# Optimization experiments

Measured on AMD Instinct MI355X. Metric: run time of the kernel, lower is better.

## Reference

```python
import jax, jax.numpy as jnp
import numpy as np

B, S, H = 2, 2048, 2048
N_HEADS = 16
HEAD_DIM = H // N_HEADS  # 128


def apply_rotary(x, cos, sin):
    # x: (B, n_heads, S, head_dim); cos/sin: (S, head_dim//2)
    d = x.shape[-1] // 2
    x1, x2 = x[..., :d], x[..., d:]
    c = cos[None, None, :x.shape[2]]
    s = sin[None, None, :x.shape[2]]
    return jnp.concatenate([x1 * c - x2 * s, x2 * c + x1 * s], axis=-1)


def setup_inputs() -> dict:
    key = jax.random.key(0)
    k1, k2, k3 = jax.random.split(key, 3)
    x = jax.random.normal(k1, (B, S, H), dtype=jnp.float32)
    qkv_w = jax.random.normal(k2, (3 * H, H), dtype=jnp.float32) * (1.0 / np.sqrt(H))
    o_w = jax.random.normal(k3, (H, H), dtype=jnp.float32) * (1.0 / np.sqrt(H))
    # rotary tables, half head_dim
    inv_freq = 1.0 / (10000.0 ** (jnp.arange(0, HEAD_DIM // 2, dtype=jnp.float32) / (HEAD_DIM // 2)))
    t = jnp.arange(S, dtype=jnp.float32)
    freqs = jnp.outer(t, inv_freq)  # (S, head_dim//2)
    cos, sin = jnp.cos(freqs), jnp.sin(freqs)
    # True = masked (strictly upper triangular)
    causal_mask = jnp.triu(jnp.ones((S, S), dtype=bool), k=1)
    return {"x": x, "qkv_w": qkv_w, "o_w": o_w, "cos": cos, "sin": sin,
            "causal_mask": causal_mask}


def reference(x, qkv_w, o_w, cos, sin, causal_mask):
    Bx, Sx, Hx = x.shape
    qkv = jnp.einsum('bsh,oh->bso', x, qkv_w)  # (B,S,3H)
    qkv = qkv.reshape(Bx, Sx, 3, N_HEADS, HEAD_DIM)
    q, k, v = qkv[:, :, 0], qkv[:, :, 1], qkv[:, :, 2]
    q = jnp.transpose(q, (0, 2, 1, 3))  # (B,nh,S,hd)
    k = jnp.transpose(k, (0, 2, 1, 3))
    v = jnp.transpose(v, (0, 2, 1, 3))
    q = apply_rotary(q, cos, sin)
    k = apply_rotary(k, cos, sin)
    scale = 1.0 / jnp.sqrt(jnp.asarray(HEAD_DIM, dtype=x.dtype))
    attn = jnp.einsum('bnqd,bnkd->bnqk', q, k) * scale
    attn = jnp.where(causal_mask[None, None], -jnp.inf, attn)
    attn = jax.nn.softmax(attn, axis=-1)
    out = jnp.einsum('bnqk,bnkd->bnqd', attn, v)
    out = jnp.transpose(out, (0, 2, 1, 3)).reshape(Bx, Sx, Hx)
    return jnp.einsum('bsh,oh->bso', out, o_w)
```

## Files before the change

kernel.cpp:

```cpp
#include <hip/hip_runtime.h>
#include <hip/hip_bf16.h>
#include <stdint.h>

typedef __attribute__((ext_vector_type(4))) float f32x4;
typedef __attribute__((ext_vector_type(8))) short s16x8;
typedef __attribute__((ext_vector_type(4))) short s16x4;

#define SWZ(g, row) ((((g) & ~7) | (((g) ^ ((row) & 7)) & 7)))

__device__ __forceinline__ unsigned short f2bf(float f) {
  unsigned u = __builtin_bit_cast(unsigned, f);
  u += 0x7fffu + ((u >> 16) & 1u);
  return (unsigned short)(u >> 16);
}

__device__ __forceinline__ void gld16(const void* g, void* l) {
  __builtin_amdgcn_global_load_lds(
      (const __attribute__((address_space(1))) void*)g,
      (__attribute__((address_space(3))) void*)l, 16, 0, 0);
}

__global__ void cvt_f32_to_bf16(const float* __restrict__ src,
                                unsigned short* __restrict__ dst, int n4) {
  int i = blockIdx.x * blockDim.x + threadIdx.x;
  if (i >= n4) return;
  float4 v = ((const float4*)src)[i];
  s16x4 o;
  o[0] = (short)f2bf(v.x); o[1] = (short)f2bf(v.y);
  o[2] = (short)f2bf(v.z); o[3] = (short)f2bf(v.w);
  ((s16x4*)dst)[i] = o;
}

#define STG(ORG, LDSB, HALF, KT) \
  gld16((const char*)((ORG) + ((size_t)((HALF)*128 + srow)) * 2048 + (size_t)(KT) * 64) + gsw, (LDSB) + (HALF) * 16384 + wid * 2048); \
  gld16((const char*)((ORG) + ((size_t)((HALF)*128 + srow + 8)) * 2048 + (size_t)(KT) * 64) + gsw, (LDSB) + (HALF) * 16384 + wid * 2048 + 1024);

#define PH(MQ, NQ, ENDWAIT, ...) \
  { s16x8 af[4][2], bv[2][2]; \
    _Pragma("unroll") for (int j = 0; j < 4; ++j) { \
      const int ra = (MQ)*128 + wm*64 + j*16 + lg; \
      _Pragma("unroll") for (int ks = 0; ks < 2; ++ks) \
        af[j][ks] = *(const s16x8*)(sAc + ra*128 + (((ks*4+hg)^(ra&7)) << 4)); } \
    _Pragma("unroll") for (int j2 = 0; j2 < 2; ++j2) { \
      const int rb = (NQ)*128 + wn*16 + j2*64 + lg; \
      _Pragma("unroll") for (int ks = 0; ks < 2; ++ks) \
        bv[j2][ks] = *(const s16x8*)(sBc + rb*128 + (((ks*4+hg)^(rb&7)) << 4)); } \
    __VA_ARGS__ \
    __builtin_amdgcn_s_barrier(); \
    asm volatile("s_waitcnt lgkmcnt(0)" ::: "memory"); \
    __builtin_amdgcn_sched_barrier(0); \
    __builtin_amdgcn_s_setprio(1); \
    _Pragma("unroll") for (int j = 0; j < 4; ++j) \
      _Pragma("unroll") for (int j2 = 0; j2 < 2; ++j2) \
        _Pragma("unroll") for (int ks = 0; ks < 2; ++ks) \
          acc[(MQ)*4+j][(NQ)*2+j2] = __builtin_amdgcn_mfma_f32_16x16x32_bf16( \
              af[j][ks], bv[j2][ks], acc[(MQ)*4+j][(NQ)*2+j2], 0, 0, 0); \
    __builtin_amdgcn_s_setprio(0); \
    ENDWAIT \
    __builtin_amdgcn_s_barrier(); }

__global__ __launch_bounds__(512, 1) void gemm_qkv_256(
    const unsigned short* __restrict__ A,
    const unsigned short* __restrict__ Bt,
    const float* __restrict__ cosT, const float* __restrict__ sinT,
    unsigned short* __restrict__ qOut, unsigned short* __restrict__ kOut,
    unsigned short* __restrict__ vtOut)
{
  __shared__ char smem[131072];
  const int tid = (int)threadIdx.x;
  const int wid = tid >> 6, l = tid & 63;
  const int lg = l & 15, hg = l >> 4;
  const int wm = wid >> 2, wn = wid & 3;
  const int s = ((int)blockIdx.x & 7) * 48 + ((int)blockIdx.x >> 3);
  const int bm0 = (s & 15) * 256, bn0 = (s >> 4) * 256;

  const int srow = wid * 16 + (l >> 3);
  const int gsw = ((l & 7) ^ (l >> 3)) << 4;

  const unsigned short* Aorg = A + (size_t)bm0 * 2048;
  const unsigned short* Borg = Bt + (size_t)bn0 * 2048;

  f32x4 acc[8][4] = {};

  STG(Aorg, smem + 0, 0, 0)
  STG(Borg, smem + 32768, 0, 0)
  STG(Borg, smem + 32768, 1, 0)
  STG(Aorg, smem + 0, 1, 0)
  asm volatile("s_waitcnt vmcnt(4)" ::: "memory");
  __builtin_amdgcn_s_barrier();

  for (int t = 0; t < 31; ++t) {
    const char* sAc = smem + (t & 1) * 65536;
    const char* sBc = sAc + 32768;
    char* dA = smem + (((t & 1) ^ 1) * 65536);
    char* dB = dA + 32768;
    PH(0, 0, asm volatile("s_waitcnt vmcnt(4)" ::: "memory");, STG(Aorg, dA, 0, t + 1))
    PH(0, 1, asm volatile("s_waitcnt vmcnt(4)" ::: "memory");, STG(Borg, dB, 0, t + 1))
    PH(1, 0, , STG(Borg, dB, 1, t + 1))
    PH(1, 1, asm volatile("s_waitcnt vmcnt(4)" ::: "memory");, STG(Aorg, dA, 1, t + 1))
  }
  {
    const char* sAc = smem + 65536;
    const char* sBc = sAc + 32768;
    PH(0, 0, asm volatile("s_waitcnt vmcnt(2)" ::: "memory");, )
    PH(0, 1, asm volatile("s_waitcnt vmcnt(0)" ::: "memory");, )
    PH(1, 0, , )
    PH(1, 1, , )
  }

  #pragma unroll
  for (int a = 0; a < 8; ++a) {
    const int gr0 = bm0 + (a >> 2) * 128 + wm * 64 + (a & 3) * 16 + hg * 4;
    #pragma unroll
    for (int pb = 0; pb < 2; ++pb) {
      const int obase = bn0 + pb * 128;
      const int tt = obase >> 11;
      const int h = (obase >> 7) & 15;
      const int d = wn * 16 + lg;
      if (tt < 2) {
        unsigned short* dst = (tt == 0) ? qOut : kOut;
        #pragma unroll
        for (int r = 0; r < 4; ++r) {
          const int gr = gr0 + r;
          const int b = gr >> 11, s1 = gr & 2047;
          const float x1 = acc[a][pb * 2 + 0][r];
          const float x2 = acc[a][pb * 2 + 1][r];
          const float cv = cosT[s1 * 64 + d];
          const float sv = sinT[s1 * 64 + d];
          const size_t base = (((size_t)b * 16 + h) * 2048 + s1) * 128;
          dst[base + d]      = f2bf(x1 * cv - x2 * sv);
          dst[base + d + 64] = f2bf(x2 * cv + x1 * sv);
        }
      } else {
        const int b = gr0 >> 11, s0 = gr0 & 2047;
        s16x4 p1, p2;
        #pragma unroll
        for (int r = 0; r < 4; ++r) {
          p1[r] = (short)f2bf(acc[a][pb * 2 + 0][r]);
          p2[r] = (short)f2bf(acc[a][pb * 2 + 1][r]);
        }
        *(s16x4*)(vtOut + (((size_t)b * 16 + h) * 128 + d)      * 2048 + s0) = p1;
        *(s16x4*)(vtOut + (((size_t)b * 16 + h) * 128 + d + 64) * 2048 + s0) = p2;
      }
    }
  }
}

template<int EPI>
__global__ __launch_bounds__(256) void gemm_bt(
    const unsigned short* __restrict__ A,
    const unsigned short* __restrict__ Bt,
    float* __restrict__ C, int N, int K)
{
  __shared__ char smem[32768];
  const int tid = (int)threadIdx.x;
  const int w  = tid >> 6, l = tid & 63;
  const int lg = l & 15, hg = l >> 4;
  const int bn0 = (int)blockIdx.x * 128, bm0 = (int)blockIdx.y * 128;

  f32x4 acc[2][8] = {};
  const int nkt = K >> 6;
  for (int kt = 0; kt < nkt; ++kt) {
    __syncthreads();
    for (int i = 0; i < 4; ++i) {
      const int G = w * 256 + i * 64 + l;
      const int row = G >> 3, g = G & 7;
      const int gs = SWZ(g, row);
      gld16((const char*)(A  + (size_t)(bm0 + row) * K + (size_t)kt * 64) + (gs << 4),
            smem + w * 4096 + i * 1024);
      gld16((const char*)(Bt + (size_t)(bn0 + row) * K + (size_t)kt * 64) + (gs << 4),
            smem + 16384 + w * 4096 + i * 1024);
    }
    asm volatile("s_waitcnt vmcnt(0)" ::: "memory");
    __syncthreads();
    for (int ks = 0; ks < 2; ++ks) {
      s16x8 af[2], bfr[8];
      for (int ai = 0; ai < 2; ++ai) {
        const int ra = w * 32 + ai * 16 + lg;
        const int gr = SWZ(4 * ks + hg, ra);
        af[ai] = *(const s16x8*)(smem + ra * 128 + (gr << 4));
      }
      for (int bi = 0; bi < 8; ++bi) {
        const int rb = bi * 16 + lg;
        const int gr = SWZ(4 * ks + hg, rb);
        bfr[bi] = *(const s16x8*)(smem + 16384 + rb * 128 + (gr << 4));
      }
      for (int ai = 0; ai < 2; ++ai)
        for (int bi = 0; bi < 8; ++bi)
          acc[ai][bi] = __builtin_amdgcn_mfma_f32_16x16x32_bf16(
              af[ai], bfr[bi], acc[ai][bi], 0, 0, 0);
    }
  }

  for (int ai = 0; ai < 2; ++ai)
    for (int bi = 0; bi < 8; ++bi) {
      const int col  = bn0 + bi * 16 + lg;
      const int row0 = bm0 + w * 32 + ai * 16 + hg * 4;
      for (int r = 0; r < 4; ++r)
        C[(size_t)(row0 + r) * N + col] = acc[ai][bi][r];
    }
}

__global__ __launch_bounds__(256) void attn_fwd(
    const unsigned short* __restrict__ Qp, const unsigned short* __restrict__ Kp,
    const unsigned short* __restrict__ Vt, unsigned short* __restrict__ AO)
{
  __shared__ char sK[16384];
  __shared__ char sV[16384];
  __shared__ char sP[8192];

  const int tid = (int)threadIdx.x, w = tid >> 6, l = tid & 63;
  const int lg = l & 15, hg = l >> 4;
  const int bid = (int)blockIdx.x;
  const int p = bid >> 8, c = bid & 255;
  const int j = c >> 5, bh = c & 31;
  const int qt = (p == 0) ? j : (p == 1) ? 31 - j : (p == 2) ? 8 + j : 23 - j;
  const size_t qkBase = (size_t)bh * 2048 * 128;
  const int qw0 = qt * 64 + w * 16;
  const int qi = qw0 + lg;

  s16x8 qf[4];
  for (int ks = 0; ks < 4; ++ks)
    qf[ks] = *(const s16x8*)(Qp + qkBase + (size_t)(qw0 + lg) * 128 + ks * 32 + hg * 8);

  f32x4 acc_o[8] = {};
  float mrun = -1e30f, lrun = 0.f;
  const float SCALE = 0.08838834764831845f;
  const float L2E = 1.4426950408889634f;
  const float CS = SCALE * L2E;

  const int nkv = qt + 1;
  for (int kv = 0; kv < nkv; ++kv) {
    const int kv0 = kv * 64;
    __syncthreads();
    for (int i = 0; i < 4; ++i) {
      const int G = w * 256 + i * 64 + l;
      const int rk = G >> 4, gk = G & 15;
      gld16((const char*)(Kp + qkBase + (size_t)(kv0 + rk) * 128) + (SWZ(gk, rk) << 4),
            sK + w * 4096 + i * 1024);
      const int rv = G >> 3, gv = G & 7;
      gld16((const char*)(Vt + qkBase + (size_t)rv * 2048 + kv0) + (SWZ(gv, rv) << 4),
            sV + w * 4096 + i * 1024);
    }
    asm volatile("s_waitcnt vmcnt(0)" ::: "memory");
    __syncthreads();

    f32x4 accs[4] = {};
    for (int ks = 0; ks < 4; ++ks)
      for (int kf = 0; kf < 4; ++kf) {
        const int row = kf * 16 + lg;
        const int g = SWZ(4 * ks + hg, row);
        s16x8 kfrag = *(const s16x8*)(sK + row * 256 + (g << 4));
        accs[kf] = __builtin_amdgcn_mfma_f32_16x16x32_bf16(kfrag, qf[ks], accs[kf], 0, 0, 0);
      }

    const bool diag = (kv == qt);
    float raw[4][4];
    float mt = -1e30f;
    #pragma unroll
    for (int kf = 0; kf < 4; ++kf)
      #pragma unroll
      for (int r = 0; r < 4; ++r) {
        float s = accs[kf][r];
        if (diag) {
          const int jj = kv0 + kf * 16 + hg * 4 + r;
          s = (jj > qi) ? -1e30f : s;
        }
        raw[kf][r] = s;
        mt = fmaxf(mt, s);
      }
    mt = fmaxf(mt, __shfl_xor(mt, 16));
    mt = fmaxf(mt, __shfl_xor(mt, 32));
    mt *= SCALE;
    if (!__all(mt - mrun <= 8.0f)) {
      const float mnew = fmaxf(mrun, mt);
      const float alpha = exp2f((mrun - mnew) * L2E);
      float ar[4];
      #pragma unroll
      for (int r = 0; r < 4; ++r) ar[r] = __shfl(alpha, hg * 4 + r);
      #pragma unroll
      for (int f = 0; f < 8; ++f)
        #pragma unroll
        for (int r = 0; r < 4; ++r) acc_o[f][r] *= ar[r];
      lrun *= alpha;
      mrun = mnew;
    }
    const float mL = mrun * L2E;
    float ls = 0.f;
    char* pw = sP + w * 2048;
    #pragma unroll
    for (int kf = 0; kf < 4; ++kf) {
      s16x4 pk;
      #pragma unroll
      for (int r = 0; r < 4; ++r) {
        const float e = exp2f(raw[kf][r] * CS - mL);
        ls += e;
        pk[r] = (short)f2bf(e);
      }
      const int j0 = kf * 16 + hg * 4;
      *(s16x4*)(pw + lg * 128 + (SWZ(j0 >> 3, lg) << 4) + ((j0 * 2) & 15)) = pk;
    }
    ls += __shfl_xor(ls, 16);
    ls += __shfl_xor(ls, 32);
    lrun += ls;
    asm volatile("" ::: "memory");

    for (int jc = 0; jc < 2; ++jc) {
      const int gp = SWZ(hg + 4 * jc, lg);
      s16x8 pa = *(const s16x8*)(pw + lg * 128 + (gp << 4));
      for (int f = 0; f < 8; ++f) {
        const int rv = f * 16 + lg;
        const int gv = SWZ(hg + 4 * jc, rv);
        s16x8 vb = *(const s16x8*)(sV + rv * 128 + (gv << 4));
        acc_o[f] = __builtin_amdgcn_mfma_f32_16x16x32_bf16(pa, vb, acc_o[f], 0, 0, 0);
      }
    }
  }

  float linv[4];
  for (int r = 0; r < 4; ++r) linv[r] = 1.0f / __shfl(lrun, hg * 4 + r);
  const int b = bh >> 4, h = bh & 15;
  for (int f = 0; f < 8; ++f) {
    const int d = h * 128 + f * 16 + lg;
    for (int r = 0; r < 4; ++r) {
      const int srow = qw0 + hg * 4 + r;
      AO[((size_t)(b * 2048 + srow)) * 2048 + d] = f2bf(acc_o[f][r] * linv[r]);
    }
  }
}

extern "C" void kernel_launch(void* const* d_in, const int* in_sizes, int n_in,
                              void* d_out, int out_size, void* d_ws, size_t ws_size,
                              hipStream_t stream) {
  const float* x    = (const float*)d_in[0];
  const float* qkvw = (const float*)d_in[1];
  const float* ow   = (const float*)d_in[2];
  const float* cosT = (const float*)d_in[3];
  const float* sinT = (const float*)d_in[4];
  float* out = (float*)d_out;

  unsigned short* X16  = (unsigned short*)d_ws;
  unsigned short* W16  = X16  + (size_t)8388608;
  unsigned short* OW16 = W16  + (size_t)12582912;
  unsigned short* Qp   = OW16 + (size_t)4194304;
  unsigned short* Kp   = Qp   + (size_t)8388608;
  unsigned short* Vtp  = Kp   + (size_t)8388608;
  unsigned short* AO   = Vtp  + (size_t)8388608;

  cvt_f32_to_bf16<<<8192, 256, 0, stream>>>(x, X16, 2097152);
  cvt_f32_to_bf16<<<12288, 256, 0, stream>>>(qkvw, W16, 3145728);
  cvt_f32_to_bf16<<<4096, 256, 0, stream>>>(ow, OW16, 1048576);

  gemm_qkv_256<<<384, 512, 0, stream>>>(X16, W16, cosT, sinT, Qp, Kp, Vtp);

  attn_fwd<<<1024, 256, 0, stream>>>(Qp, Kp, Vtp, AO);

  dim3 g2(16, 32);
  gemm_bt<0><<<g2, 256, 0, stream>>>(AO, OW16, out, 2048, 2048);
}
```

Baseline: 277.6 us.

## Retile QKV GEMM to 128x384 blocks with simpler double-buffered pipeline

Changes the QKV projection GEMM tile from 256x256 to 128x384 (three head-dim column groups per block), launching 512 blocks instead of 384 on 512 threads each. The fine-grained four-phase interleaving of loads and MFMAs is replaced by a single stage-next-tile-then-compute loop with one wait and two barriers per K step. The aim is to fill the CUs more evenly, since 512 blocks spread across 256 CUs more cleanly than 384. The cost is lower arithmetic intensity per tile and less overlap between loads and compute within a K step.

```diff
diff --git a/kernel.cpp b/kernel.cpp
--- a/kernel.cpp
+++ b/kernel.cpp
@@ -31,35 +31,31 @@
   ((s16x4*)dst)[i] = o;
 }
 
-#define STG(ORG, LDSB, HALF, KT) \
-  gld16((const char*)((ORG) + ((size_t)((HALF)*128 + srow)) * 2048 + (size_t)(KT) * 64) + gsw, (LDSB) + (HALF) * 16384 + wid * 2048); \
-  gld16((const char*)((ORG) + ((size_t)((HALF)*128 + srow + 8)) * 2048 + (size_t)(KT) * 64) + gsw, (LDSB) + (HALF) * 16384 + wid * 2048 + 1024);
-
-#define PH(MQ, NQ, ENDWAIT, ...) \
-  { s16x8 af[4][2], bv[2][2]; \
+#define STAGE384(BB, KT) \
+  { char* dA = smem + (BB) * 65536; \
+    char* dB = dA + 16384; \
+    _Pragma("unroll") for (int rr = 0; rr < 2; ++rr) { \
+      const int G = rr * 512 + tid; const int row = G >> 3, g = G & 7; \
+      gld16((const char*)(Aorg + (size_t)row * 2048 + (size_t)(KT) * 64) + (SWZ(g, row) << 4), \
+            dA + rr * 8192 + tid * 16); } \
+    _Pragma("unroll") for (int rr = 0; rr < 6; ++rr) { \
+      const int G = rr * 512 + tid; const int row = G >> 3, g = G & 7; \
+      gld16((const char*)(Borg + (size_t)row * 2048 + (size_t)(KT) * 64) + (SWZ(g, row) << 4), \
+            dB + rr * 8192 + tid * 16); } }
+
+#define CPH384(KS) \
+  { s16x8 av[4], bv[6]; \
     _Pragma("unroll") for (int j = 0; j < 4; ++j) { \
-      const int ra = (MQ)*128 + wm*64 + j*16 + lg; \
-      _Pragma("unroll") for (int ks = 0; ks < 2; ++ks) \
-        af[j][ks] = *(const s16x8*)(sAc + ra*128 + (((ks*4+hg)^(ra&7)) << 4)); } \
-    _Pragma("unroll") for (int j2 = 0; j2 < 2; ++j2) { \
-      const int rb = (NQ)*128 + wn*16 + j2*64 + lg; \
-      _Pragma("unroll") for (int ks = 0; ks < 2; ++ks) \
-        bv[j2][ks] = *(const s16x8*)(sBc + rb*128 + (((ks*4+hg)^(rb&7)) << 4)); } \
-    __VA_ARGS__ \
-    __builtin_amdgcn_s_barrier(); \
-    asm volatile("s_waitcnt lgkmcnt(0)" ::: "memory"); \
-    __builtin_amdgcn_sched_barrier(0); \
-    __builtin_amdgcn_s_setprio(1); \
+      const int ra = wm * 64 + j * 16 + lg; \
+      av[j] = *(const s16x8*)(sA + ra * 128 + (SWZ(4 * (KS) + hg, ra) << 4)); } \
+    _Pragma("unroll") for (int b = 0; b < 6; ++b) { \
+      const int cb = (b >> 1) * 128 + wn * 16 + (b & 1) * 64 + lg; \
+      bv[b] = *(const s16x8*)(sB + cb * 128 + (SWZ(4 * (KS) + hg, cb) << 4)); } \
     _Pragma("unroll") for (int j = 0; j < 4; ++j) \
-      _Pragma("unroll") for (int j2 = 0; j2 < 2; ++j2) \
-        _Pragma("unroll") for (int ks = 0; ks < 2; ++ks) \
-          acc[(MQ)*4+j][(NQ)*2+j2] = __builtin_amdgcn_mfma_f32_16x16x32_bf16( \
-              af[j][ks], bv[j2][ks], acc[(MQ)*4+j][(NQ)*2+j2], 0, 0, 0); \
-    __builtin_amdgcn_s_setprio(0); \
-    ENDWAIT \
-    __builtin_amdgcn_s_barrier(); }
-
-__global__ __launch_bounds__(512, 1) void gemm_qkv_256(
+      _Pragma("unroll") for (int b = 0; b < 6; ++b) \
+        acc[j][b] = __builtin_amdgcn_mfma_f32_16x16x32_bf16(av[j], bv[b], acc[j][b], 0, 0, 0); }
+
+__global__ __launch_bounds__(512, 1) void gemm_qkv_384(
     const unsigned short* __restrict__ A,
     const unsigned short* __restrict__ Bt,
     const float* __restrict__ cosT, const float* __restrict__ sinT,
@@ -71,76 +67,73 @@
   const int wid = tid >> 6, l = tid & 63;
   const int lg = l & 15, hg = l >> 4;
   const int wm = wid >> 2, wn = wid & 3;
-  const int s = ((int)blockIdx.x & 7) * 48 + ((int)blockIdx.x >> 3);
-  const int bm0 = (s & 15) * 256, bn0 = (s >> 4) * 256;
-
-  const int srow = wid * 16 + (l >> 3);
-  const int gsw = ((l & 7) ^ (l >> 3)) << 4;
+  const int s = ((int)blockIdx.x & 7) * 64 + ((int)blockIdx.x >> 3);
+  const int bm0 = (s & 31) * 128, bn0 = (s >> 5) * 384;
 
   const unsigned short* Aorg = A + (size_t)bm0 * 2048;
   const unsigned short* Borg = Bt + (size_t)bn0 * 2048;
 
-  f32x4 acc[8][4] = {};
-
-  STG(Aorg, smem + 0, 0, 0)
-  STG(Borg, smem + 32768, 0, 0)
-  STG(Borg, smem + 32768, 1, 0)
-  STG(Aorg, smem + 0, 1, 0)
-  asm volatile("s_waitcnt vmcnt(4)" ::: "memory");
-  __builtin_amdgcn_s_barrier();
-
+  f32x4 acc[4][6] = {};
+
+  STAGE384(0, 0)
   for (int t = 0; t < 31; ++t) {
-    const char* sAc = smem + (t & 1) * 65536;
-    const char* sBc = sAc + 32768;
-    char* dA = smem + (((t & 1) ^ 1) * 65536);
-    char* dB = dA + 32768;
-    PH(0, 0, asm volatile("s_waitcnt vmcnt(4)" ::: "memory");, STG(Aorg, dA, 0, t + 1))
-    PH(0, 1, asm volatile("s_waitcnt vmcnt(4)" ::: "memory");, STG(Borg, dB, 0, t + 1))
-    PH(1, 0, , STG(Borg, dB, 1, t + 1))
-    PH(1, 1, asm volatile("s_waitcnt vmcnt(4)" ::: "memory");, STG(Aorg, dA, 1, t + 1))
+    STAGE384((t & 1) ^ 1, t + 1)
+    asm volatile("s_waitcnt vmcnt(8)" ::: "memory");
+    __builtin_amdgcn_s_barrier();
+    asm volatile("" ::: "memory");
+    const char* sA = smem + (t & 1) * 65536;
+    const char* sB = sA + 16384;
+    __builtin_amdgcn_s_setprio(1);
+    CPH384(0)
+    CPH384(1)
+    __builtin_amdgcn_s_setprio(0);
+    asm volatile("" ::: "memory");
+    __builtin_amdgcn_s_barrier();
+    asm volatile("" ::: "memory");
   }
   {
-    const char* sAc = smem + 65536;
-    const char* sBc = sAc + 32768;
-    PH(0, 0, asm volatile("s_waitcnt vmcnt(2)" ::: "memory");, )
-    PH(0, 1, asm volatile("s_waitcnt vmcnt(0)" ::: "memory");, )
-    PH(1, 0, , )
-    PH(1, 1, , )
+    asm volatile("s_waitcnt vmcnt(0)" ::: "memory");
+    __builtin_amdgcn_s_barrier();
+    asm volatile("" ::: "memory");
+    const char* sA = smem + 65536;
+    const char* sB = sA + 16384;
+    CPH384(0)
+    CPH384(1)
   }
 
   #pragma unroll
-  for (int a = 0; a < 8; ++a) {
-    const int gr0 = bm0 + (a >> 2) * 128 + wm * 64 + (a & 3) * 16 + hg * 4;
+  for (int j = 0; j < 4; ++j) {
+    const int grow0 = bm0 + wm * 64 + j * 16 + hg * 4;
+    const int b_ = grow0 >> 11;
     #pragma unroll
-    for (int pb = 0; pb < 2; ++pb) {
-      const int obase = bn0 + pb * 128;
-      const int tt = obase >> 11;
-      const int h = (obase >> 7) & 15;
+    for (int cg = 0; cg < 3; ++cg) {
+      const int og = (bn0 >> 7) + cg;
+      const int tt = og >> 4, h = og & 15;
       const int d = wn * 16 + lg;
       if (tt < 2) {
         unsigned short* dst = (tt == 0) ? qOut : kOut;
         #pragma unroll
         for (int r = 0; r < 4; ++r) {
-          const int gr = gr0 + r;
-          const int b = gr >> 11, s1 = gr & 2047;
-          const float x1 = acc[a][pb * 2 + 0][r];
-          const float x2 = acc[a][pb * 2 + 1][r];
+          const int gr = grow0 + r;
+          const int s1 = gr & 2047;
+          const float x1 = acc[j][cg * 2 + 0][r];
+          const float x2 = acc[j][cg * 2 + 1][r];
           const float cv = cosT[s1 * 64 + d];
           const float sv = sinT[s1 * 64 + d];
-          const size_t base = (((size_t)b * 16 + h) * 2048 + s1) * 128;
+          const size_t base = (((size_t)b_ * 16 + h) * 2048 + s1) * 128;
           dst[base + d]      = f2bf(x1 * cv - x2 * sv);
           dst[base + d + 64] = f2bf(x2 * cv + x1 * sv);
         }
       } else {
-        const int b = gr0 >> 11, s0 = gr0 & 2047;
+        const int s0 = grow0 & 2047;
         s16x4 p1, p2;
         #pragma unroll
         for (int r = 0; r < 4; ++r) {
-          p1[r] = (short)f2bf(acc[a][pb * 2 + 0][r]);
-          p2[r] = (short)f2bf(acc[a][pb * 2 + 1][r]);
+          p1[r] = (short)f2bf(acc[j][cg * 2 + 0][r]);
+          p2[r] = (short)f2bf(acc[j][cg * 2 + 1][r]);
         }
-        *(s16x4*)(vtOut + (((size_t)b * 16 + h) * 128 + d)      * 2048 + s0) = p1;
-        *(s16x4*)(vtOut + (((size_t)b * 16 + h) * 128 + d + 64) * 2048 + s0) = p2;
+        *(s16x4*)(vtOut + (((size_t)b_ * 16 + h) * 128 + d)      * 2048 + s0) = p1;
+        *(s16x4*)(vtOut + (((size_t)b_ * 16 + h) * 128 + d + 64) * 2048 + s0) = p2;
       }
     }
   }
@@ -351,7 +344,7 @@
   cvt_f32_to_bf16<<<12288, 256, 0, stream>>>(qkvw, W16, 3145728);
   cvt_f32_to_bf16<<<4096, 256, 0, stream>>>(ow, OW16, 1048576);
 
-  gemm_qkv_256<<<384, 512, 0, stream>>>(X16, W16, cosT, sinT, Qp, Kp, Vtp);
+  gemm_qkv_384<<<512, 512, 0, stream>>>(X16, W16, cosT, sinT, Qp, Kp, Vtp);
 
   attn_fwd<<<1024, 256, 0, stream>>>(Qp, Kp, Vtp, AO);
 
```

Measured after the change: 251.6 us. 1.1x faster.
